# Optimization experiments

Hardware: AMD Instinct MI355X
Metric: run time of the kernel (lower is better)

The kernel has to match this reference:

```python
import jax, jax.numpy as jnp
import numpy as np

PATCHSIZE = 7
STRIDE = 3
PADDING = (3, 3, 3, 3)  # top, bottom, left, right


def _fold(xp, k, stride):
    """col2im: scatter-add patches [B,C,k,k,nH,nW] -> image [B,C,H,W]."""
    B, C, _, _, nH, nW = xp.shape
    H = (nH - 1) * stride + k
    W = (nW - 1) * stride + k
    out = jnp.zeros((B, C, H, W), dtype=xp.dtype)
    # loop over the small, static k*k kernel offsets; each add is a strided
    # scatter covering the full patch grid (vectorized over B,C,nH,nW)
    for i in range(k):
        for j in range(k):
            out = out.at[:, :, i:i + stride * nH:stride,
                         j:j + stride * nW:stride].add(xp[:, :, i, j])
    return out


def setup_inputs() -> dict:
    key = jax.random.key(0)
    x_patch = jax.random.normal(key, (4, 64, 7, 7, 85, 85), dtype=jnp.float32)
    return {"x_patch": x_patch}


def reference(x_patch) -> jnp.ndarray:
    k, stride = PATCHSIZE, STRIDE
    padtop, padbottom, padleft, padright = PADDING
    counts = _fold(jnp.ones_like(x_patch), k, stride)
    x = _fold(x_patch, k, stride)
    x = x / counts
    H, W = x.shape[2], x.shape[3]
    return x[:, :, padtop:H - padbottom, padleft:W - padright]
```

## Files before the change

kernel.cpp:

```cpp
#include <hip/hip_runtime.h>


constexpr int K   = 7;
constexpr int S   = 3;
constexpr int NH  = 85;
constexpr int NW  = 85;
constexpr int OH  = 253;
constexpr int OW  = 253;
constexpr int PAD = 3;

__global__ __launch_bounds__(256) void patch2im_kernel(
    const float* __restrict__ x, float* __restrict__ out, int total)
{
    int idx = blockIdx.x * 256 + threadIdx.x;
    if (idx >= total) return;

    int w  = idx % OW;
    int t  = idx / OW;
    int h  = t % OH;
    int bc = t / OH;

    int hp = h + PAD;
    int wp = w + PAD;

    int ph_min = (hp - (K - 1) + (S - 1)) / S;
    if (ph_min < 0) ph_min = 0;
    int ph_max = hp / S;
    if (ph_max > NH - 1) ph_max = NH - 1;

    int pw_min = (wp - (K - 1) + (S - 1)) / S;
    if (pw_min < 0) pw_min = 0;
    int pw_max = wp / S;
    if (pw_max > NW - 1) pw_max = NW - 1;

    int nh = ph_max - ph_min + 1;
    int nw = pw_max - pw_min + 1;

    const float* base = x + (long long)bc * (K * K * NH * NW);

    float sum = 0.0f;
    #pragma unroll 3
    for (int ph = ph_min; ph <= ph_max; ++ph) {
        int i = hp - S * ph;
        const float* rowb = base + (i * K) * (NH * NW) + ph * NW;
        #pragma unroll 3
        for (int pw = pw_min; pw <= pw_max; ++pw) {
            int j = wp - S * pw;
            sum += rowb[j * (NH * NW) + pw];
        }
    }

    out[idx] = sum / (float)(nh * nw);
}

extern "C" void kernel_launch(void* const* d_in, const int* in_sizes, int n_in,
                              void* d_out, int out_size, void* d_ws, size_t ws_size,
                              hipStream_t stream) {
    const float* x = (const float*)d_in[0];
    float* out = (float*)d_out;

    int total = out_size;
    int blocks = (total + 255) / 256;
    patch2im_kernel<<<blocks, 256, 0, stream>>>(x, out, total);
}
```

Baseline: 592.7 us.

## Compute three output columns per thread with coalesced per-patch loads

Each thread now produces three adjacent output pixels (one stride period) instead of one. The inner column loop is replaced by explicit loads indexed by patch column t, so consecutive threads read consecutive addresses within each kernel-offset plane. Three accumulators are reused across patch rows, and the thread count drops by about 3x. This is meant to cut redundant index arithmetic and scattered loads, at the cost of hardcoding the B*C=256 and stride-3 geometry in the launch and in the boundary handling.

```diff
diff --git a/kernel.cpp b/kernel.cpp
--- a/kernel.cpp
+++ b/kernel.cpp
@@ -8,6 +8,8 @@
 constexpr int OH  = 253;
 constexpr int OW  = 253;
 constexpr int PAD = 3;
+constexpr int PLANE = NH * NW;
+constexpr int TQ  = 85;
 
 __global__ __launch_bounds__(256) void patch2im_kernel(
     const float* __restrict__ x, float* __restrict__ out, int total)
@@ -15,42 +17,51 @@
     int idx = blockIdx.x * 256 + threadIdx.x;
     if (idx >= total) return;
 
-    int w  = idx % OW;
-    int t  = idx / OW;
-    int h  = t % OH;
-    int bc = t / OH;
+    int t  = idx % TQ;
+    int r2 = idx / TQ;
+    int h  = r2 % OH;
+    int bc = r2 / OH;
 
+    int q  = t + 1;
     int hp = h + PAD;
-    int wp = w + PAD;
 
-    int ph_min = (hp - (K - 1) + (S - 1)) / S;
-    if (ph_min < 0) ph_min = 0;
+    int ph_min = (hp >= K) ? (hp - (K - 1) + (S - 1)) / S : 0;
     int ph_max = hp / S;
     if (ph_max > NH - 1) ph_max = NH - 1;
+    int nh = ph_max - ph_min + 1;
 
-    int pw_min = (wp - (K - 1) + (S - 1)) / S;
-    if (pw_min < 0) pw_min = 0;
-    int pw_max = wp / S;
-    if (pw_max > NW - 1) pw_max = NW - 1;
+    const bool hasR = (q <= NW - 1);
+    const bool hasL = (t >= 1);
 
-    int nh = ph_max - ph_min + 1;
-    int nw = pw_max - pw_min + 1;
+    const float* base = x + (size_t)bc * (K * K * PLANE);
 
-    const float* base = x + (long long)bc * (K * K * NH * NW);
-
-    float sum = 0.0f;
-    #pragma unroll 3
+    float o0 = 0.f, o1 = 0.f, o2 = 0.f;
     for (int ph = ph_min; ph <= ph_max; ++ph) {
         int i = hp - S * ph;
-        const float* rowb = base + (i * K) * (NH * NW) + ph * NW;
-        #pragma unroll 3
-        for (int pw = pw_min; pw <= pw_max; ++pw) {
-            int j = wp - S * pw;
-            sum += rowb[j * (NH * NW) + pw];
-        }
+        const float* pb = base + (i * K) * PLANE + ph * NW;
+        float v3 = pb[3 * PLANE + t];
+        float v4 = pb[4 * PLANE + t];
+        float v5 = pb[5 * PLANE + t];
+        float v0 = hasR ? pb[0 * PLANE + q] : 0.f;
+        float v1 = hasR ? pb[1 * PLANE + q] : 0.f;
+        float v2 = hasR ? pb[2 * PLANE + q] : 0.f;
+        float v6 = hasL ? pb[6 * PLANE + (t - 1)] : 0.f;
+        o0 += v0 + v3 + v6;
+        o1 += v1 + v4;
+        o2 += v2 + v5;
     }
 
-    out[idx] = sum / (float)(nh * nw);
+    int nw0 = 1 + (hasR ? 1 : 0) + (hasL ? 1 : 0);
+    float fnh = (float)nh;
+
+    float* orow = out + ((size_t)bc * OH + h) * OW;
+    int w0 = 3 * t;
+    orow[w0] = o0 / (fnh * (float)nw0);
+    if (t < TQ - 1) {
+        float inv = 1.0f / (fnh * 2.0f);
+        orow[w0 + 1] = o1 * inv;
+        orow[w0 + 2] = o2 * inv;
+    }
 }
 
 extern "C" void kernel_launch(void* const* d_in, const int* in_sizes, int n_in,
@@ -59,7 +70,7 @@
     const float* x = (const float*)d_in[0];
     float* out = (float*)d_out;
 
-    int total = out_size;
+    int total = 256 * OH * TQ;
     int blocks = (total + 255) / 256;
     patch2im_kernel<<<blocks, 256, 0, stream>>>(x, out, total);
 }
```

Result: faster. 482.4 us (-18.6%).

## Compute 12 output columns per thread with vectorized float4 patch loads

Applied to the files above, without the earlier changes.

Each thread now handles one output row and a chunk of four patch columns (twelve output pixels). It loads seven contiguous float4 vectors from the patch planes per patch row and accumulates by output phase. Divisors are replaced by precomputed reciprocals based on edge position. The goal is to cut scalar gather loads and index arithmetic, at the cost of misaligned vector loads, reads that can fall outside a row at the edges (masked afterwards), and strided output stores. The grid size is hardcoded to B*C=256.

```diff
diff --git a/kernel.cpp b/kernel.cpp
--- a/kernel.cpp
+++ b/kernel.cpp
@@ -8,6 +8,12 @@
 constexpr int OH  = 253;
 constexpr int OW  = 253;
 constexpr int PAD = 3;
+constexpr int PLANE  = NH * NW;
+constexpr int CHUNKS = 22;
+
+__device__ __forceinline__ void ld4(float* dst, const float* p) {
+    __builtin_memcpy(dst, p, 16);
+}
 
 __global__ __launch_bounds__(256) void patch2im_kernel(
     const float* __restrict__ x, float* __restrict__ out, int total)
@@ -15,42 +21,68 @@
     int idx = blockIdx.x * 256 + threadIdx.x;
     if (idx >= total) return;
 
-    int w  = idx % OW;
-    int t  = idx / OW;
-    int h  = t % OH;
-    int bc = t / OH;
+    int tt = idx % CHUNKS;
+    int r2 = idx / CHUNKS;
+    int h  = r2 % OH;
+    int bc = r2 / OH;
 
+    int t0 = 4 * tt;
     int hp = h + PAD;
-    int wp = w + PAD;
 
-    int ph_min = (hp - (K - 1) + (S - 1)) / S;
-    if (ph_min < 0) ph_min = 0;
+    int ph_min = (hp >= K) ? (hp - (K - 1) + (S - 1)) / S : 0;
     int ph_max = hp / S;
     if (ph_max > NH - 1) ph_max = NH - 1;
+    int nh = ph_max - ph_min + 1;
 
-    int pw_min = (wp - (K - 1) + (S - 1)) / S;
-    if (pw_min < 0) pw_min = 0;
-    int pw_max = wp / S;
-    if (pw_max > NW - 1) pw_max = NW - 1;
+    const float* base = x + (size_t)bc * (K * K * PLANE);
 
-    int nh = ph_max - ph_min + 1;
-    int nw = pw_max - pw_min + 1;
+    float m6 = (tt == 0)          ? 0.f : 1.f;
+    float m0 = (tt == CHUNKS - 1) ? 0.f : 1.f;
 
-    const float* base = x + (long long)bc * (K * K * NH * NW);
+    float o0[4] = {0.f, 0.f, 0.f, 0.f};
+    float o1[4] = {0.f, 0.f, 0.f, 0.f};
+    float o2[4] = {0.f, 0.f, 0.f, 0.f};
 
-    float sum = 0.0f;
-    #pragma unroll 3
     for (int ph = ph_min; ph <= ph_max; ++ph) {
         int i = hp - S * ph;
-        const float* rowb = base + (i * K) * (NH * NW) + ph * NW;
-        #pragma unroll 3
-        for (int pw = pw_min; pw <= pw_max; ++pw) {
-            int j = wp - S * pw;
-            sum += rowb[j * (NH * NW) + pw];
+        const float* pb = base + (i * K) * PLANE + ph * NW;
+
+        float a0[4], a1[4], a2[4], a3[4], a4[4], a5[4], a6[4];
+        ld4(a0, pb + 0 * PLANE + t0 + 1);
+        ld4(a1, pb + 1 * PLANE + t0 + 1);
+        ld4(a2, pb + 2 * PLANE + t0 + 1);
+        ld4(a3, pb + 3 * PLANE + t0);
+        ld4(a4, pb + 4 * PLANE + t0);
+        ld4(a5, pb + 5 * PLANE + t0);
+        ld4(a6, pb + 6 * PLANE + t0 - 1);
+
+        a6[0] *= m6;
+        a0[0] *= m0;
+
+        #pragma unroll
+        for (int e = 0; e < 4; ++e) {
+            o0[e] += a0[e] + a3[e] + a6[e];
+            o1[e] += a1[e] + a4[e];
+            o2[e] += a2[e] + a5[e];
         }
     }
 
-    out[idx] = sum / (float)(nh * nw);
+    float inv2 = (nh == 3) ? (1.f / 6.f) : (1.f / 4.f);
+    float inv3 = (nh == 3) ? (1.f / 9.f) : (1.f / 6.f);
+
+    float* orow = out + ((size_t)bc * OH + h) * OW + 3 * t0;
+
+    #pragma unroll
+    for (int e = 0; e < 4; ++e) {
+        int t = t0 + e;
+        if (t > NW - 1) break;
+        bool edge = (t == 0) | (t == NW - 1);
+        orow[3 * e] = o0[e] * (edge ? inv2 : inv3);
+        if (t < NW - 1) {
+            orow[3 * e + 1] = o1[e] * inv2;
+            orow[3 * e + 2] = o2[e] * inv2;
+        }
+    }
 }
 
 extern "C" void kernel_launch(void* const* d_in, const int* in_sizes, int n_in,
@@ -59,7 +91,7 @@
     const float* x = (const float*)d_in[0];
     float* out = (float*)d_out;
 
-    int total = out_size;
+    int total = 256 * OH * CHUNKS;
     int blocks = (total + 255) / 256;
     patch2im_kernel<<<blocks, 256, 0, stream>>>(x, out, total);
 }
```

After: 484.9 us. 18.2% less time.

## Stage patch rows in LDS and compute three output columns per thread by phase

Applied to the files above, without the earlier changes.

Replaces the one-thread-per-output gather with blocks that each own one output-row phase (h mod 3) and a band of 8 patch rows. Each block first loads the needed kernel-offset planes into shared memory with coalesced reads, then each thread accumulates three adjacent output pixels and divides by precomputed overlap counts. The aim is to cut redundant, scattered global reads and the per-pixel index arithmetic. It hardcodes batch*channel = 256 in the launch and depends on fairly intricate boundary masking, so it is fragile to any change in shape.

```diff
diff --git a/kernel.cpp b/kernel.cpp
--- a/kernel.cpp
+++ b/kernel.cpp
@@ -1,56 +1,92 @@
 #include <hip/hip_runtime.h>
 
 
-constexpr int K   = 7;
-constexpr int S   = 3;
-constexpr int NH  = 85;
-constexpr int NW  = 85;
-constexpr int OH  = 253;
-constexpr int OW  = 253;
-constexpr int PAD = 3;
+constexpr int NW    = 85;
+constexpr int OH    = 253, OW = 253;
+constexpr int PLANE = 85 * 85;
+constexpr int P     = 8;
+constexpr int MB    = 11;
+constexpr int PSTR  = P * NW;
 
 __global__ __launch_bounds__(256) void patch2im_kernel(
-    const float* __restrict__ x, float* __restrict__ out, int total)
+    const float* __restrict__ x, float* __restrict__ out)
 {
-    int idx = blockIdx.x * 256 + threadIdx.x;
-    if (idx >= total) return;
+    __shared__ float lds[21 * PSTR];
 
-    int w  = idx % OW;
-    int t  = idx / OW;
-    int h  = t % OH;
-    int bc = t / OH;
+    int bid = blockIdx.x;
+    int mb  = bid % MB;
+    int t1  = bid / MB;
+    int c   = t1 % 3;
+    int bc  = t1 / 3;
 
-    int hp = h + PAD;
-    int wp = w + PAD;
+    int m0    = 1 + P * mb;
+    int nd    = (c == 0) ? 3 : 2;
+    int m_max = (c == 0) ? 85 : 84;
 
-    int ph_min = (hp - (K - 1) + (S - 1)) / S;
-    if (ph_min < 0) ph_min = 0;
-    int ph_max = hp / S;
-    if (ph_max > NH - 1) ph_max = NH - 1;
+    const float* __restrict__ base = x + (size_t)bc * (49 * PLANE);
 
-    int pw_min = (wp - (K - 1) + (S - 1)) / S;
-    if (pw_min < 0) pw_min = 0;
-    int pw_max = wp / S;
-    if (pw_max > NW - 1) pw_max = NW - 1;
+    int total = nd * 7 * PSTR;
+    for (int u = threadIdx.x; u < total; u += 256) {
+        int pw = u % NW;
+        int r  = u / NW;
+        int mm = r & (P - 1);
+        int pl = r / P;
+        int d  = pl / 7;
+        int j  = pl - 7 * d;
+        int ph = m0 + mm - d;
+        ph = min(max(ph, 0), 84);
+        lds[u] = base[((c + 3 * d) * 7 + j) * PLANE + ph * NW + pw];
+    }
+    __syncthreads();
 
-    int nh = ph_max - ph_min + 1;
-    int nw = pw_max - pw_min + 1;
+#define ACC(DD, FD)                                                       \
+    {                                                                     \
+        const float* L = lds + (DD * 7) * PSTR + mm * NW;                 \
+        float v0 = L[0 * PSTR + tp], v1 = L[1 * PSTR + tp],               \
+              v2 = L[2 * PSTR + tp], v3 = L[3 * PSTR + t],                \
+              v4 = L[4 * PSTR + t],  v5 = L[5 * PSTR + t],                \
+              v6 = L[6 * PSTR + tm];                                      \
+        o0 += (FD) * (v0 * mR + v3 + v6 * mL);                            \
+        o1 += (FD) * (v1 * mR + v4);                                      \
+        o2 += (FD) * (v2 * mR + v5);                                      \
+    }
 
-    const float* base = x + (long long)bc * (K * K * NH * NW);
+    for (int u = threadIdx.x; u < PSTR; u += 256) {
+        int t  = u % NW;
+        int mm = u / NW;
+        int m  = m0 + mm;
+        if (m > m_max) continue;
 
-    float sum = 0.0f;
-    #pragma unroll 3
-    for (int ph = ph_min; ph <= ph_max; ++ph) {
-        int i = hp - S * ph;
-        const float* rowb = base + (i * K) * (NH * NW) + ph * NW;
-        #pragma unroll 3
-        for (int pw = pw_min; pw <= pw_max; ++pw) {
-            int j = wp - S * pw;
-            sum += rowb[j * (NH * NW) + pw];
+        float mR = (t <= 83) ? 1.f : 0.f;
+        float mL = (t >= 1)  ? 1.f : 0.f;
+        int   tp = min(t + 1, 84);
+        int   tm = max(t - 1, 0);
+
+        float f0 = (m <= 84) ? 1.f : 0.f;
+        float o0 = 0.f, o1 = 0.f, o2 = 0.f;
+        ACC(0, f0)
+        ACC(1, 1.f)
+        bool nh3 = false;
+        if (c == 0) {
+            float f2 = (m >= 2) ? 1.f : 0.f;
+            ACC(2, f2)
+            nh3 = (f0 != 0.f) && (f2 != 0.f);
+        }
+
+        float inv2 = nh3 ? (1.f / 6.f) : (1.f / 4.f);
+        bool  nw3  = (t >= 1) && (t <= 83);
+        float inv0 = nh3 ? (nw3 ? (1.f / 9.f) : (1.f / 6.f))
+                         : (nw3 ? (1.f / 6.f) : (1.f / 4.f));
+
+        int h = 3 * m + c - 3;
+        float* orow = out + ((size_t)bc * OH + h) * OW + 3 * t;
+        orow[0] = o0 * inv0;
+        if (t < 84) {
+            orow[1] = o1 * inv2;
+            orow[2] = o2 * inv2;
         }
     }
-
-    out[idx] = sum / (float)(nh * nw);
+#undef ACC
 }
 
 extern "C" void kernel_launch(void* const* d_in, const int* in_sizes, int n_in,
@@ -59,7 +95,6 @@
     const float* x = (const float*)d_in[0];
     float* out = (float*)d_out;
 
-    int total = out_size;
-    int blocks = (total + 255) / 256;
-    patch2im_kernel<<<blocks, 256, 0, stream>>>(x, out, total);
+    int blocks = 256 * 3 * MB;
+    patch2im_kernel<<<blocks, 256, 0, stream>>>(x, out);
 }
```

Measured after the change: 590.9 us. About the same (-0.3%).
